# Performance work log

Hardware: AMD Instinct MI355X
Metric: run time of the kernel (lower is better)

## Reference

```python
import jax, jax.numpy as jnp
import numpy as np

LMBDA = 1.0  # undefined 'lmbda' in source; treated as hyperparameter = 1.0


def _entropy(logits):
    # entropy of softmax(logits) along last axis: -(p * log p).sum(-1)
    logp = jax.nn.log_softmax(logits, axis=-1)
    return -jnp.sum(jnp.exp(logp) * logp, axis=-1)


def setup_inputs() -> dict:
    key = jax.random.key(0)
    T, M, K = 4096, 64, 256
    block_feats = jax.random.normal(key, (T, M * K), dtype=jnp.float32)
    return {"block_feats": block_feats, "M": M}


def reference(block_feats, M):
    T, MK = block_feats.shape
    K = MK // M
    blocks = block_feats.reshape(T, M, K)  # chunk along dim=1 -> [T, M, K]

    # Mean Entropy Loss: per-sample, per-block entropy, averaged over blocks then batch
    L1 = jnp.mean(_entropy(blocks))  # mean over T and M

    # Batch Entropy Loss: entropy of the batch-mean logits per block
    block_mean = jnp.mean(blocks, axis=0)  # [M, K]
    L2 = -jnp.mean(_entropy(block_mean))   # -sum2 / M

    return L1 + LMBDA * L2
```

## Files before the change

kernel.cpp:

```cpp
#include <hip/hip_runtime.h>

#define T_DIM 4096
#define M_DIM 64
#define K_DIM 256
#define CHUNKS 128
#define ROWS_PER_WAVE (T_DIM / CHUNKS)

__global__ __launch_bounds__(256) void cluster_pass1(
    const float4* __restrict__ x,
    float* __restrict__ colsum,
    float* __restrict__ hsum)
{
    const int wave = threadIdx.x >> 6;
    const int lane = threadIdx.x & 63;
    const int m_group = blockIdx.x & 15;
    const int chunk   = blockIdx.x >> 4;
    const int m  = m_group * 4 + wave;
    const int t0 = chunk * ROWS_PER_WAVE;

    const float4* p = x + (size_t)t0 * (M_DIM * K_DIM / 4) + m * (K_DIM / 4) + lane;

    float cs0 = 0.f, cs1 = 0.f, cs2 = 0.f, cs3 = 0.f;
    float hacc = 0.f;

    for (int i = 0; i < ROWS_PER_WAVE; ++i, p += (M_DIM * K_DIM / 4)) {
        const float4 v = *p;

        cs0 += v.x; cs1 += v.y; cs2 += v.z; cs3 += v.w;

        const float e0 = __expf(v.x), e1 = __expf(v.y),
                    e2 = __expf(v.z), e3 = __expf(v.w);
        float s = (e0 + e1) + (e2 + e3);
        float d = (v.x * e0 + v.y * e1) + (v.z * e2 + v.w * e3);

        #pragma unroll
        for (int off = 32; off >= 1; off >>= 1) {
            s += __shfl_xor(s, off, 64);
            d += __shfl_xor(d, off, 64);
        }
        hacc += __logf(s) - d / s;
    }

    float* col = colsum + m * K_DIM + lane * 4;
    atomicAdd(col + 0, cs0);
    atomicAdd(col + 1, cs1);
    atomicAdd(col + 2, cs2);
    atomicAdd(col + 3, cs3);

    __shared__ float lds[4];
    if (lane == 0) lds[wave] = hacc;
    __syncthreads();
    if (threadIdx.x == 0)
        atomicAdd(hsum, (lds[0] + lds[1]) + (lds[2] + lds[3]));
}

__global__ __launch_bounds__(256) void cluster_pass2(
    const float* __restrict__ colsum,
    const float* __restrict__ hsum,
    float* __restrict__ out)
{
    const int wave = threadIdx.x >> 6;
    const int lane = threadIdx.x & 63;
    const float invT = 1.0f / (float)T_DIM;

    float eacc = 0.f;
    for (int m = wave; m < M_DIM; m += 4) {
        const float* row = colsum + m * K_DIM + lane * 4;
        const float v0 = row[0] * invT, v1 = row[1] * invT,
                    v2 = row[2] * invT, v3 = row[3] * invT;
        const float e0 = __expf(v0), e1 = __expf(v1),
                    e2 = __expf(v2), e3 = __expf(v3);
        float s = (e0 + e1) + (e2 + e3);
        float d = (v0 * e0 + v1 * e1) + (v2 * e2 + v3 * e3);
        #pragma unroll
        for (int off = 32; off >= 1; off >>= 1) {
            s += __shfl_xor(s, off, 64);
            d += __shfl_xor(d, off, 64);
        }
        eacc += __logf(s) - d / s;
    }

    __shared__ float lds[4];
    if (lane == 0) lds[wave] = eacc;
    __syncthreads();
    if (threadIdx.x == 0) {
        const float e2sum = (lds[0] + lds[1]) + (lds[2] + lds[3]);
        const float L1 = hsum[0] * (1.0f / (float)(T_DIM * M_DIM));
        const float L2 = -e2sum * (1.0f / (float)M_DIM);
        out[0] = L1 + L2;
    }
}

extern "C" void kernel_launch(void* const* d_in, const int* in_sizes, int n_in,
                              void* d_out, int out_size, void* d_ws, size_t ws_size,
                              hipStream_t stream) {
    const float* x = (const float*)d_in[0];
    float* ws = (float*)d_ws;
    float* colsum = ws;
    float* hsum   = ws + M_DIM * K_DIM;

    hipMemsetAsync(d_ws, 0, (M_DIM * K_DIM + 1) * sizeof(float), stream);

    cluster_pass1<<<dim3(16 * CHUNKS), dim3(256), 0, stream>>>(
        (const float4*)x, colsum, hsum);
    cluster_pass2<<<dim3(1), dim3(256), 0, stream>>>(colsum, hsum, (float*)d_out);
}
```

Baseline: 396.3 us.

## Remap wave to process four rows at once with 16-lane swizzle reductions

Each wave now splits into four 16-lane groups that each handle a different row, with every lane loading four float4s (a contiguous 64-byte run) per row. The per-row softmax sums are reduced with ds_swizzle within 16 lanes instead of a full 64-lane shuffle tree. Column sums are combined across the groups before the atomics, cutting the shuffle count per row and raising bytes in flight per load. The cost is more registers for sixteen column accumulators and per-lane accesses that are less contiguous across the wave.

```diff
diff --git a/kernel.cpp b/kernel.cpp
--- a/kernel.cpp
+++ b/kernel.cpp
@@ -4,7 +4,13 @@
 #define M_DIM 64
 #define K_DIM 256
 #define CHUNKS 128
-#define ROWS_PER_WAVE (T_DIM / CHUNKS)
+#define ROWS_PER_WAVE 32
+#define QUADS (ROWS_PER_WAVE / 4)
+
+template <int PAT>
+__device__ __forceinline__ float swz_add(float v) {
+    return v + __int_as_float(__builtin_amdgcn_ds_swizzle(__float_as_int(v), PAT));
+}
 
 __global__ __launch_bounds__(256) void cluster_pass1(
     const float4* __restrict__ x,
@@ -13,39 +19,74 @@
 {
     const int wave = threadIdx.x >> 6;
     const int lane = threadIdx.x & 63;
+    const int g    = lane >> 4;
+    const int sl   = lane & 15;
     const int m_group = blockIdx.x & 15;
     const int chunk   = blockIdx.x >> 4;
     const int m  = m_group * 4 + wave;
     const int t0 = chunk * ROWS_PER_WAVE;
 
-    const float4* p = x + (size_t)t0 * (M_DIM * K_DIM / 4) + m * (K_DIM / 4) + lane;
+    const float4* base = x + (size_t)(t0 + g) * (M_DIM * K_DIM / 4)
+                           + m * (K_DIM / 4) + sl * 4;
+    const size_t quad_stride = (size_t)4 * (M_DIM * K_DIM / 4);
 
-    float cs0 = 0.f, cs1 = 0.f, cs2 = 0.f, cs3 = 0.f;
+    float cs[16];
+    #pragma unroll
+    for (int j = 0; j < 16; ++j) cs[j] = 0.f;
     float hacc = 0.f;
 
-    for (int i = 0; i < ROWS_PER_WAVE; ++i, p += (M_DIM * K_DIM / 4)) {
-        const float4 v = *p;
+    #pragma unroll 2
+    for (int q = 0; q < QUADS; ++q) {
+        const float4* p = base + q * quad_stride;
+        const float4 v0 = p[0], v1 = p[1], v2 = p[2], v3 = p[3];
 
-        cs0 += v.x; cs1 += v.y; cs2 += v.z; cs3 += v.w;
+        cs[0]  += v0.x; cs[1]  += v0.y; cs[2]  += v0.z; cs[3]  += v0.w;
+        cs[4]  += v1.x; cs[5]  += v1.y; cs[6]  += v1.z; cs[7]  += v1.w;
+        cs[8]  += v2.x; cs[9]  += v2.y; cs[10] += v2.z; cs[11] += v2.w;
+        cs[12] += v3.x; cs[13] += v3.y; cs[14] += v3.z; cs[15] += v3.w;
 
-        const float e0 = __expf(v.x), e1 = __expf(v.y),
-                    e2 = __expf(v.z), e3 = __expf(v.w);
-        float s = (e0 + e1) + (e2 + e3);
-        float d = (v.x * e0 + v.y * e1) + (v.z * e2 + v.w * e3);
+        float s = 0.f, d = 0.f;
+        {
+            float e;
+            e = __expf(v0.x); s += e; d += v0.x * e;
+            e = __expf(v0.y); s += e; d += v0.y * e;
+            e = __expf(v0.z); s += e; d += v0.z * e;
+            e = __expf(v0.w); s += e; d += v0.w * e;
+            e = __expf(v1.x); s += e; d += v1.x * e;
+            e = __expf(v1.y); s += e; d += v1.y * e;
+            e = __expf(v1.z); s += e; d += v1.z * e;
+            e = __expf(v1.w); s += e; d += v1.w * e;
+            e = __expf(v2.x); s += e; d += v2.x * e;
+            e = __expf(v2.y); s += e; d += v2.y * e;
+            e = __expf(v2.z); s += e; d += v2.z * e;
+            e = __expf(v2.w); s += e; d += v2.w * e;
+            e = __expf(v3.x); s += e; d += v3.x * e;
+            e = __expf(v3.y); s += e; d += v3.y * e;
+            e = __expf(v3.z); s += e; d += v3.z * e;
+            e = __expf(v3.w); s += e; d += v3.w * e;
+        }
 
-        #pragma unroll
-        for (int off = 32; off >= 1; off >>= 1) {
-            s += __shfl_xor(s, off, 64);
-            d += __shfl_xor(d, off, 64);
-        }
+        s = swz_add<0x041F>(s); d = swz_add<0x041F>(d);
+        s = swz_add<0x081F>(s); d = swz_add<0x081F>(d);
+        s = swz_add<0x101F>(s); d = swz_add<0x101F>(d);
+        s = swz_add<0x201F>(s); d = swz_add<0x201F>(d);
+
         hacc += __logf(s) - d / s;
     }
 
-    float* col = colsum + m * K_DIM + lane * 4;
-    atomicAdd(col + 0, cs0);
-    atomicAdd(col + 1, cs1);
-    atomicAdd(col + 2, cs2);
-    atomicAdd(col + 3, cs3);
+    #pragma unroll
+    for (int j = 0; j < 16; ++j) {
+        cs[j] = swz_add<0x401F>(cs[j]);
+        cs[j] += __shfl_xor(cs[j], 32, 64);
+    }
+    if (g == 0) {
+        float* col = colsum + m * K_DIM + sl * 16;
+        #pragma unroll
+        for (int j = 0; j < 16; ++j) atomicAdd(col + j, cs[j]);
+    }
+
+    hacc = swz_add<0x401F>(hacc);
+    hacc += __shfl_xor(hacc, 32, 64);
 
     __shared__ float lds[4];
     if (lane == 0) lds[wave] = hacc;
@@ -99,7 +140,7 @@
     float* colsum = ws;
     float* hsum   = ws + M_DIM * K_DIM;
 
-    hipMemsetAsync(d_ws, 0, (M_DIM * K_DIM + 1) * sizeof(float), stream);
+    (void)hipMemsetAsync(d_ws, 0, (M_DIM * K_DIM + 1) * sizeof(float), stream);
 
     cluster_pass1<<<dim3(16 * CHUNKS), dim3(256), 0, stream>>>(
         (const float4*)x, colsum, hsum);
```

Result: slower. 447.4 us (+12.9%).

## Replace atomics with partial-sum buffers and LDS-batched row reductions

Applied to the files above, without the earlier changes.

The first pass no longer uses global float atomics for column sums. Each chunk writes a float4 partial to a workspace, a new middle kernel sums the 128 chunk partials per column, and a final kernel reduces the per-block entropy partials. Per-row wave reductions (12 cross-lane shuffles per row) are replaced by staging 8 rows of (s,d) in LDS, letting 8-lane groups sum them and finishing with ds_swizzle, which amortises the reduction across rows. The cost is an extra kernel launch plus roughly 8 MB of partial writes and re-reads, and the hacc scaling now relies on each row's entropy being counted 8 times.

```diff
diff --git a/kernel.cpp b/kernel.cpp
--- a/kernel.cpp
+++ b/kernel.cpp
@@ -4,68 +4,114 @@
 #define M_DIM 64
 #define K_DIM 256
 #define CHUNKS 128
-#define ROWS_PER_WAVE (T_DIM / CHUNKS)
+#define ROWS 32
+#define PASS_ROWS 8
+#define NPASS (ROWS / PASS_ROWS)
+#define ROW_STRIDE (M_DIM * K_DIM / 4)
+
+#define ROW_F2 66
+#define WAVE_F2 (PASS_ROWS * ROW_F2)
+
+template <int PAT>
+__device__ __forceinline__ float swz_add(float v) {
+    return v + __int_as_float(__builtin_amdgcn_ds_swizzle(__float_as_int(v), PAT));
+}
 
 __global__ __launch_bounds__(256) void cluster_pass1(
     const float4* __restrict__ x,
-    float* __restrict__ colsum,
-    float* __restrict__ hsum)
+    float4* __restrict__ part,
+    float* __restrict__ hpart)
 {
+    __shared__ float2 lds[4 * WAVE_F2];
+    __shared__ float harr[4];
+
     const int wave = threadIdx.x >> 6;
     const int lane = threadIdx.x & 63;
-    const int m_group = blockIdx.x & 15;
-    const int chunk   = blockIdx.x >> 4;
-    const int m  = m_group * 4 + wave;
-    const int t0 = chunk * ROWS_PER_WAVE;
+    const int g = lane >> 3;
+    const int j = lane & 7;
+    const int mg    = blockIdx.x & 15;
+    const int chunk = blockIdx.x >> 4;
+    const int m  = mg * 4 + wave;
+    const int t0 = chunk * ROWS;
 
-    const float4* p = x + (size_t)t0 * (M_DIM * K_DIM / 4) + m * (K_DIM / 4) + lane;
+    const float4* base = x + (size_t)t0 * ROW_STRIDE + m * (K_DIM / 4) + lane;
+    float2* wl = lds + wave * WAVE_F2;
 
     float cs0 = 0.f, cs1 = 0.f, cs2 = 0.f, cs3 = 0.f;
     float hacc = 0.f;
 
-    for (int i = 0; i < ROWS_PER_WAVE; ++i, p += (M_DIM * K_DIM / 4)) {
-        const float4 v = *p;
-
-        cs0 += v.x; cs1 += v.y; cs2 += v.z; cs3 += v.w;
-
-        const float e0 = __expf(v.x), e1 = __expf(v.y),
-                    e2 = __expf(v.z), e3 = __expf(v.w);
-        float s = (e0 + e1) + (e2 + e3);
-        float d = (v.x * e0 + v.y * e1) + (v.z * e2 + v.w * e3);
-
+    for (int p = 0; p < NPASS; ++p) {
         #pragma unroll
-        for (int off = 32; off >= 1; off >>= 1) {
-            s += __shfl_xor(s, off, 64);
-            d += __shfl_xor(d, off, 64);
+        for (int r = 0; r < PASS_ROWS; ++r) {
+            const float4 v = base[(size_t)(p * PASS_ROWS + r) * ROW_STRIDE];
+            cs0 += v.x; cs1 += v.y; cs2 += v.z; cs3 += v.w;
+            const float e0 = __expf(v.x), e1 = __expf(v.y),
+                        e2 = __expf(v.z), e3 = __expf(v.w);
+            const float s = (e0 + e1) + (e2 + e3);
+            const float d = (v.x * e0 + v.y * e1) + (v.z * e2 + v.w * e3);
+            wl[r * ROW_F2 + lane] = make_float2(s, d);
         }
+        float s = 0.f, d = 0.f;
+        #pragma unroll
+        for (int u = 0; u < 8; ++u) {
+            const float2 t = wl[g * ROW_F2 + j * 8 + u];
+            s += t.x; d += t.y;
+        }
+        s = swz_add<0x041F>(s); d = swz_add<0x041F>(d);
+        s = swz_add<0x081F>(s); d = swz_add<0x081F>(d);
+        s = swz_add<0x101F>(s); d = swz_add<0x101F>(d);
         hacc += __logf(s) - d / s;
     }
 
-    float* col = colsum + m * K_DIM + lane * 4;
-    atomicAdd(col + 0, cs0);
-    atomicAdd(col + 1, cs1);
-    atomicAdd(col + 2, cs2);
-    atomicAdd(col + 3, cs3);
+    part[(size_t)chunk * (M_DIM * K_DIM / 4) + m * (K_DIM / 4) + lane] =
+        make_float4(cs0, cs1, cs2, cs3);
 
-    __shared__ float lds[4];
-    if (lane == 0) lds[wave] = hacc;
+    hacc = swz_add<0x041F>(hacc);
+    hacc = swz_add<0x081F>(hacc);
+    hacc = swz_add<0x101F>(hacc);
+    hacc = swz_add<0x201F>(hacc);
+    hacc = swz_add<0x401F>(hacc);
+    hacc += __shfl_xor(hacc, 32, 64);
+
+    if (lane == 0) harr[wave] = hacc;
     __syncthreads();
     if (threadIdx.x == 0)
-        atomicAdd(hsum, (lds[0] + lds[1]) + (lds[2] + lds[3]));
+        hpart[blockIdx.x] = (harr[0] + harr[1]) + (harr[2] + harr[3]);
 }
 
 __global__ __launch_bounds__(256) void cluster_pass2(
-    const float* __restrict__ colsum,
-    const float* __restrict__ hsum,
+    const float* __restrict__ part,
+    float* __restrict__ colred)
+{
+    const int f = blockIdx.x * 256 + threadIdx.x;
+    float a = 0.f;
+    #pragma unroll 8
+    for (int c = 0; c < CHUNKS; ++c)
+        a += part[(size_t)c * (M_DIM * K_DIM) + f];
+    colred[f] = a;
+}
+
+__global__ __launch_bounds__(256) void cluster_pass3(
+    const float* __restrict__ colred,
+    const float* __restrict__ hpart,
     float* __restrict__ out)
 {
     const int wave = threadIdx.x >> 6;
     const int lane = threadIdx.x & 63;
+
+    float h = 0.f;
+    for (int i = threadIdx.x; i < 16 * CHUNKS; i += 256) h += hpart[i];
+    h = swz_add<0x041F>(h);
+    h = swz_add<0x081F>(h);
+    h = swz_add<0x101F>(h);
+    h = swz_add<0x201F>(h);
+    h = swz_add<0x401F>(h);
+    h += __shfl_xor(h, 32, 64);
+
     const float invT = 1.0f / (float)T_DIM;
-
     float eacc = 0.f;
     for (int m = wave; m < M_DIM; m += 4) {
-        const float* row = colsum + m * K_DIM + lane * 4;
+        const float* row = colred + m * K_DIM + lane * 4;
         const float v0 = row[0] * invT, v1 = row[1] * invT,
                     v2 = row[2] * invT, v3 = row[3] * invT;
         const float e0 = __expf(v0), e1 = __expf(v1),
@@ -80,13 +126,14 @@
         eacc += __logf(s) - d / s;
     }
 
-    __shared__ float lds[4];
-    if (lane == 0) lds[wave] = eacc;
+    __shared__ float lh[4], le[4];
+    if (lane == 0) { lh[wave] = h; le[wave] = eacc; }
     __syncthreads();
     if (threadIdx.x == 0) {
-        const float e2sum = (lds[0] + lds[1]) + (lds[2] + lds[3]);
-        const float L1 = hsum[0] * (1.0f / (float)(T_DIM * M_DIM));
-        const float L2 = -e2sum * (1.0f / (float)M_DIM);
+        const float Hs = (lh[0] + lh[1]) + (lh[2] + lh[3]);
+        const float Es = (le[0] + le[1]) + (le[2] + le[3]);
+        const float L1 = Hs * (1.0f / (8.0f * (float)T_DIM * (float)M_DIM));
+        const float L2 = -Es * (1.0f / (float)M_DIM);
         out[0] = L1 + L2;
     }
 }
@@ -96,12 +143,14 @@
                               hipStream_t stream) {
     const float* x = (const float*)d_in[0];
     float* ws = (float*)d_ws;
-    float* colsum = ws;
-    float* hsum   = ws + M_DIM * K_DIM;
-
-    hipMemsetAsync(d_ws, 0, (M_DIM * K_DIM + 1) * sizeof(float), stream);
+    float* part   = ws;
+    float* hpart  = ws + (size_t)CHUNKS * M_DIM * K_DIM;
+    float* colred = hpart + 16 * CHUNKS;
 
     cluster_pass1<<<dim3(16 * CHUNKS), dim3(256), 0, stream>>>(
-        (const float4*)x, colsum, hsum);
-    cluster_pass2<<<dim3(1), dim3(256), 0, stream>>>(colsum, hsum, (float*)d_out);
+        (const float4*)x, (float4*)part, hpart);
+    cluster_pass2<<<dim3(M_DIM * K_DIM / 256), dim3(256), 0, stream>>>(
+        part, colred);
+    cluster_pass3<<<dim3(1), dim3(256), 0, stream>>>(
+        colred, hpart, (float*)d_out);
 }
```

New measurement: 378.4 us. 1.05x faster.
